# Performance work log

Hardware: AMD Instinct MI355X
Metric: run time of the kernel (lower is better)

## Reference

```python
import jax, jax.numpy as jnp
import numpy as np

N, E, F, B = 4096, 8192, 256, 16


def setup_inputs() -> dict:
    key = jax.random.key(0)
    k_x, k_idx, k_w, k_b = jax.random.split(key, 4)
    x = jax.random.normal(k_x, (B, E, F), dtype=jnp.float32)
    # Incidence matrix: each edge (column) connects 2 random distinct nodes.
    ends = jax.random.randint(k_idx, (2, E), 0, N)  # [2, E] node ids per edge
    cols = jnp.arange(E)
    inci = jnp.zeros((N, E), dtype=jnp.float32)
    inci = inci.at[ends[0], cols].set(1.0).at[ends[1], cols].set(1.0)
    w = jax.random.normal(k_w, (N, E), dtype=jnp.float32) * 0.05
    b = jax.random.normal(k_b, (N, E), dtype=jnp.float32) * 0.01
    return {"x": x, "inci": inci, "w": w, "b": b}


def reference(x, inci, w, b):
    # (w * inci + b) @ x : [N,E] x [B,E,F] -> [B,N,F]
    m = w * inci + b
    return jnp.einsum("ne,bef->bnf", m, x)
```

## Files before the change

kernel.cpp:

```cpp
#include <hip/hip_runtime.h>
#include <hip/hip_bf16.h>

#define Ndim 4096
#define Edim 8192
#define Fdim 256
#define Bdim 16
#define EB (Edim * 2)
#define NT (Edim / 64)

typedef __attribute__((ext_vector_type(8))) short bf16x8;
typedef __attribute__((ext_vector_type(4))) float f32x4;

__device__ __forceinline__ unsigned short f2bf(float f) {
  unsigned int u = __float_as_uint(f);
  u += 0x7fffu + ((u >> 16) & 1u);
  return (unsigned short)(u >> 16);
}

__device__ __forceinline__ void gload_lds16(const void* g, void* l) {
  __builtin_amdgcn_global_load_lds(
      (const __attribute__((address_space(1))) unsigned int*)g,
      (__attribute__((address_space(3))) unsigned int*)l, 16, 0, 0);
}

__device__ __forceinline__ void stage_half(const char* g, char* d) {
  gload_lds16(g, d);
  gload_lds16(g + (size_t)64 * EB, d + 8192);
}

#define RD(base, r, kk) \
  (*(const bf16x8*)((base) + (r) * 128 + ((((kk) * 64) + khi) ^ (((r) & 7) << 4))))

__global__ void convert_m(const float* __restrict__ w, const float* __restrict__ inc,
                          const float* __restrict__ bb, unsigned short* __restrict__ m) {
  size_t i = ((size_t)blockIdx.x * 256 + threadIdx.x) * 4;
  float4 wv = *(const float4*)(w + i);
  float4 iv = *(const float4*)(inc + i);
  float4 bv = *(const float4*)(bb + i);
  ushort4 o;
  o.x = f2bf(fmaf(wv.x, iv.x, bv.x));
  o.y = f2bf(fmaf(wv.y, iv.y, bv.y));
  o.z = f2bf(fmaf(wv.z, iv.z, bv.z));
  o.w = f2bf(fmaf(wv.w, iv.w, bv.w));
  *(ushort4*)(m + i) = o;
}

__global__ void transpose_x(const float* __restrict__ x, unsigned short* __restrict__ xT) {
  __shared__ unsigned short tile[64][66];
  int e0 = blockIdx.x * 64, f0 = blockIdx.y * 64, b = blockIdx.z;
  const float* xb = x + (size_t)b * Edim * Fdim;
  unsigned short* xTb = xT + (size_t)b * Fdim * Edim;
  int t = threadIdx.x;
  int fl = t & 63, rq = t >> 6;
#pragma unroll
  for (int i = 0; i < 16; i++) {
    int el = rq * 16 + i;
    float v = xb[(size_t)(e0 + el) * Fdim + f0 + fl];
    tile[el][fl] = f2bf(v);
  }
  __syncthreads();
  int ep = (t & 31) * 2;
  int fr0 = t >> 5;
#pragma unroll
  for (int j = 0; j < 8; j++) {
    int fr = fr0 + j * 8;
    unsigned int pk = (unsigned int)tile[ep][fr] | ((unsigned int)tile[ep + 1][fr] << 16);
    *(unsigned int*)&xTb[(size_t)(f0 + fr) * Edim + e0 + ep] = pk;
  }
}

template <bool S1, bool S2, bool S3, bool S4, int VM>
__device__ __forceinline__ void ktile(
    const char* lA, const char* lB,
    char* d1, const char* g1, char* d2, const char* g2,
    char* d3, const char* g3, char* d4, const char* g4,
    int lane, int wr, int wc, f32x4 acc[8][4]) {
  const int l15 = lane & 15;
  const int khi = (lane >> 4) << 4;
  bf16x8 aLo[8], aHi[8], bLo[4], bHi[4];

#pragma unroll
  for (int m = 0; m < 4; ++m)
#pragma unroll
    for (int kk = 0; kk < 2; ++kk)
      aLo[m * 2 + kk] = RD(lA, wr * 128 + m * 16 + l15, kk);
#pragma unroll
  for (int n = 0; n < 2; ++n)
#pragma unroll
    for (int kk = 0; kk < 2; ++kk)
      bLo[n * 2 + kk] = RD(lB, wc * 64 + n * 16 + l15, kk);
  if constexpr (S1) stage_half(g1, d1);
  asm volatile("s_waitcnt lgkmcnt(8)" ::: "memory");
  __builtin_amdgcn_s_barrier();
  asm volatile("s_waitcnt lgkmcnt(0)" ::: "memory");
  __builtin_amdgcn_s_setprio(1);
#pragma unroll
  for (int m = 0; m < 4; ++m)
#pragma unroll
    for (int n = 0; n < 2; ++n)
#pragma unroll
      for (int kk = 0; kk < 2; ++kk)
        acc[m][n] = __builtin_amdgcn_mfma_f32_16x16x32_bf16(aLo[m * 2 + kk], bLo[n * 2 + kk],
                                                            acc[m][n], 0, 0, 0);
  __builtin_amdgcn_s_setprio(0);
  __builtin_amdgcn_s_barrier();

#pragma unroll
  for (int n = 0; n < 2; ++n)
#pragma unroll
    for (int kk = 0; kk < 2; ++kk)
      bHi[n * 2 + kk] = RD(lB, wc * 64 + (n + 2) * 16 + l15, kk);
  if constexpr (S2) stage_half(g2, d2);
  __builtin_amdgcn_s_barrier();
  asm volatile("s_waitcnt lgkmcnt(0)" ::: "memory");
  __builtin_amdgcn_s_setprio(1);
#pragma unroll
  for (int m = 0; m < 4; ++m)
#pragma unroll
    for (int n = 0; n < 2; ++n)
#pragma unroll
      for (int kk = 0; kk < 2; ++kk)
        acc[m][n + 2] = __builtin_amdgcn_mfma_f32_16x16x32_bf16(aLo[m * 2 + kk], bHi[n * 2 + kk],
                                                                acc[m][n + 2], 0, 0, 0);
  __builtin_amdgcn_s_setprio(0);
  __builtin_amdgcn_s_barrier();

#pragma unroll
  for (int m = 0; m < 4; ++m)
#pragma unroll
    for (int kk = 0; kk < 2; ++kk)
      aHi[m * 2 + kk] = RD(lA, wr * 128 + 64 + m * 16 + l15, kk);
  if constexpr (S3) stage_half(g3, d3);
  __builtin_amdgcn_s_barrier();
  asm volatile("s_waitcnt lgkmcnt(0)" ::: "memory");
  __builtin_amdgcn_s_setprio(1);
#pragma unroll
  for (int m = 0; m < 4; ++m)
#pragma unroll
    for (int n = 0; n < 2; ++n)
#pragma unroll
      for (int kk = 0; kk < 2; ++kk)
        acc[m + 4][n] = __builtin_amdgcn_mfma_f32_16x16x32_bf16(aHi[m * 2 + kk], bLo[n * 2 + kk],
                                                                acc[m + 4][n], 0, 0, 0);
  __builtin_amdgcn_s_setprio(0);
  __builtin_amdgcn_s_barrier();

  if constexpr (S4) stage_half(g4, d4);
  __builtin_amdgcn_s_barrier();
  __builtin_amdgcn_s_setprio(1);
#pragma unroll
  for (int m = 0; m < 4; ++m)
#pragma unroll
    for (int n = 0; n < 2; ++n)
#pragma unroll
      for (int kk = 0; kk < 2; ++kk)
        acc[m + 4][n + 2] = __builtin_amdgcn_mfma_f32_16x16x32_bf16(aHi[m * 2 + kk], bHi[n * 2 + kk],
                                                                    acc[m + 4][n + 2], 0, 0, 0);
  __builtin_amdgcn_s_setprio(0);
  if constexpr (VM == 4) asm volatile("s_waitcnt vmcnt(4)" ::: "memory");
  if constexpr (VM == 0) asm volatile("s_waitcnt vmcnt(0)" ::: "memory");
  __builtin_amdgcn_s_barrier();
}

__global__ __launch_bounds__(512, 2) void gemm8(
    const unsigned short* __restrict__ A,
    const unsigned short* __restrict__ Bt,
    float* __restrict__ C) {
  __shared__ __align__(16) char smem[131072];

  const int bid = blockIdx.x;
  const int lid = ((bid & 7) << 5) | (bid >> 3);
  const int mt = lid >> 4;
  const int bb = lid & 15;

  const int tid = threadIdx.x;
  const int lane = tid & 63;
  const int w = tid >> 6;
  const int wr = w >> 2;
  const int wc = w & 3;

  const int r0 = tid >> 3;
  const int c0 = ((tid & 7) ^ (r0 & 7)) << 4;

  const char* Ag = (const char*)A + (size_t)(mt * 256) * EB + (size_t)r0 * EB + c0;
  const char* Bg = (const char*)Bt + (size_t)(bb * 256) * EB + (size_t)r0 * EB + c0;
  char* dst = smem + tid * 16;

  f32x4 acc[8][4];
#pragma unroll
  for (int m = 0; m < 8; ++m)
#pragma unroll
    for (int n = 0; n < 4; ++n) acc[m][n] = (f32x4){0.f, 0.f, 0.f, 0.f};

  const size_t HEB = (size_t)128 * EB;

  stage_half(Ag, dst);
  stage_half(Ag + HEB, dst + 16384);
  stage_half(Bg, dst + 32768);
  stage_half(Bg + HEB, dst + 49152);
  stage_half(Bg + 128, dst + 98304);
  stage_half(Bg + 128 + HEB, dst + 114688);
  asm volatile("s_waitcnt vmcnt(4)" ::: "memory");
  __builtin_amdgcn_s_barrier();

  for (int i = 0; i < NT / 2 - 1; ++i) {
    const size_t t1b = (size_t)(2 * i + 1) * 128;
    const size_t t2b = (size_t)(2 * i + 2) * 128;
    const size_t t3b = (size_t)(2 * i + 3) * 128;
    ktile<1, 1, 1, 1, 4>(smem, smem + 32768,
                         dst + 65536, Ag + t1b,
                         dst + 81920, Ag + t1b + HEB,
                         dst + 32768, Bg + t2b,
                         dst + 49152, Bg + t2b + HEB,
                         lane, wr, wc, acc);
    ktile<1, 1, 1, 1, 4>(smem + 65536, smem + 98304,
                         dst, Ag + t2b,
                         dst + 16384, Ag + t2b + HEB,
                         dst + 98304, Bg + t3b,
                         dst + 114688, Bg + t3b + HEB,
                         lane, wr, wc, acc);
  }
  {
    const size_t tlb = (size_t)(NT - 1) * 128;
    ktile<1, 1, 0, 0, 0>(smem, smem + 32768,
                         dst + 65536, Ag + tlb,
                         dst + 81920, Ag + tlb + HEB,
                         nullptr, nullptr, nullptr, nullptr,
                         lane, wr, wc, acc);
    ktile<0, 0, 0, 0, -1>(smem + 65536, smem + 98304,
                          nullptr, nullptr, nullptr, nullptr,
                          nullptr, nullptr, nullptr, nullptr,
                          lane, wr, wc, acc);
  }

  float* Cb = C + (size_t)bb * (Ndim * Fdim) + (size_t)(mt * 256) * Fdim;
#pragma unroll
  for (int m = 0; m < 8; ++m) {
    int row0 = wr * 128 + m * 16 + ((lane >> 4) << 2);
#pragma unroll
    for (int n = 0; n < 4; ++n) {
      int col = wc * 64 + n * 16 + (lane & 15);
#pragma unroll
      for (int j = 0; j < 4; ++j)
        Cb[(size_t)(row0 + j) * Fdim + col] = acc[m][n][j];
    }
  }
}

__global__ void naive_kernel(const float* __restrict__ x, const float* __restrict__ inci,
                             const float* __restrict__ w, const float* __restrict__ b,
                             float* __restrict__ out) {
  int n = blockIdx.x & (Ndim - 1);
  int bb = blockIdx.x >> 12;
  int f = threadIdx.x;
  const float* xb = x + (size_t)bb * Edim * Fdim;
  const size_t nE = (size_t)n * Edim;
  float acc = 0.f;
  for (int e = 0; e < Edim; e++) {
    float m = fmaf(w[nE + e], inci[nE + e], b[nE + e]);
    acc = fmaf(m, xb[(size_t)e * Fdim + f], acc);
  }
  out[(size_t)bb * Ndim * Fdim + (size_t)n * Fdim + f] = acc;
}

extern "C" void kernel_launch(void* const* d_in, const int* in_sizes, int n_in,
                              void* d_out, int out_size, void* d_ws, size_t ws_size,
                              hipStream_t stream) {
  const float* x = (const float*)d_in[0];
  const float* inci = (const float*)d_in[1];
  const float* w = (const float*)d_in[2];
  const float* b = (const float*)d_in[3];
  float* out = (float*)d_out;

  size_t mBytes = (size_t)Ndim * Edim * 2;
  size_t xTBytes = (size_t)Bdim * Fdim * Edim * 2;
  if (ws_size >= mBytes + xTBytes) {
    unsigned short* m_bf = (unsigned short*)d_ws;
    unsigned short* xT = m_bf + (size_t)Ndim * Edim;
    convert_m<<<(Ndim * (size_t)Edim) / 4 / 256, 256, 0, stream>>>(w, inci, b, m_bf);
    transpose_x<<<dim3(Edim / 64, Fdim / 64, Bdim), 256, 0, stream>>>(x, xT);
    gemm8<<<256, 512, 0, stream>>>(m_bf, xT, out);
  } else {
    naive_kernel<<<Bdim * Ndim, 256, 0, stream>>>(x, inci, w, b, out);
  }
}
```

Baseline: 334.4 us.

## Prefetch next tile's A fragments into registers across ktile boundaries

Restructures the per-tile GEMM pipeline so the low half of A for the next K-tile is read from LDS during the last MFMA phase of the current tile and carried in registers. The B low/high fragments are now loaded together up front, and the explicit lgkmcnt waits are dropped in favour of compiler-managed waits. The vmcnt waits are also moved earlier. The goal is to hide LDS read latency behind MFMA work and to cut stalls at phase boundaries, at the cost of more live VGPRs and a reordered barrier/stage schedule that could expose new hazards.

```diff
diff --git a/kernel.cpp b/kernel.cpp
--- a/kernel.cpp
+++ b/kernel.cpp
@@ -30,6 +30,8 @@
 
 #define RD(base, r, kk) \
   (*(const bf16x8*)((base) + (r) * 128 + ((((kk) * 64) + khi) ^ (((r) & 7) << 4))))
+
+#define BAR() do { __builtin_amdgcn_s_barrier(); asm volatile("" ::: "memory"); } while (0)
 
 __global__ void convert_m(const float* __restrict__ w, const float* __restrict__ inc,
                           const float* __restrict__ bb, unsigned short* __restrict__ m) {
@@ -69,70 +71,61 @@
   }
 }
 
-template <bool S1, bool S2, bool S3, bool S4, int VM>
+template <int MODE>
 __device__ __forceinline__ void ktile(
-    const char* lA, const char* lB,
+    const char* lA, const char* lB, const char* lAn,
     char* d1, const char* g1, char* d2, const char* g2,
     char* d3, const char* g3, char* d4, const char* g4,
-    int lane, int wr, int wc, f32x4 acc[8][4]) {
+    int lane, int wr, int wc, bf16x8 (&aCur)[8], f32x4 acc[8][4]) {
   const int l15 = lane & 15;
   const int khi = (lane >> 4) << 4;
-  bf16x8 aLo[8], aHi[8], bLo[4], bHi[4];
-
-#pragma unroll
-  for (int m = 0; m < 4; ++m)
-#pragma unroll
-    for (int kk = 0; kk < 2; ++kk)
-      aLo[m * 2 + kk] = RD(lA, wr * 128 + m * 16 + l15, kk);
+  bf16x8 bLo[4], bHi[4], aHi[8];
+
+  if constexpr (MODE >= 1) stage_half(g1, d1);
+  BAR();
 #pragma unroll
   for (int n = 0; n < 2; ++n)
 #pragma unroll
     for (int kk = 0; kk < 2; ++kk)
       bLo[n * 2 + kk] = RD(lB, wc * 64 + n * 16 + l15, kk);
-  if constexpr (S1) stage_half(g1, d1);
-  asm volatile("s_waitcnt lgkmcnt(8)" ::: "memory");
-  __builtin_amdgcn_s_barrier();
-  asm volatile("s_waitcnt lgkmcnt(0)" ::: "memory");
-  __builtin_amdgcn_s_setprio(1);
-#pragma unroll
-  for (int m = 0; m < 4; ++m)
-#pragma unroll
-    for (int n = 0; n < 2; ++n)
-#pragma unroll
-      for (int kk = 0; kk < 2; ++kk)
-        acc[m][n] = __builtin_amdgcn_mfma_f32_16x16x32_bf16(aLo[m * 2 + kk], bLo[n * 2 + kk],
+#pragma unroll
+  for (int n = 0; n < 2; ++n)
+#pragma unroll
+    for (int kk = 0; kk < 2; ++kk)
+      bHi[n * 2 + kk] = RD(lB, wc * 64 + (n + 2) * 16 + l15, kk);
+  __builtin_amdgcn_s_setprio(1);
+#pragma unroll
+  for (int m = 0; m < 4; ++m)
+#pragma unroll
+    for (int n = 0; n < 2; ++n)
+#pragma unroll
+      for (int kk = 0; kk < 2; ++kk)
+        acc[m][n] = __builtin_amdgcn_mfma_f32_16x16x32_bf16(aCur[m * 2 + kk], bLo[n * 2 + kk],
                                                             acc[m][n], 0, 0, 0);
   __builtin_amdgcn_s_setprio(0);
-  __builtin_amdgcn_s_barrier();
-
-#pragma unroll
-  for (int n = 0; n < 2; ++n)
-#pragma unroll
-    for (int kk = 0; kk < 2; ++kk)
-      bHi[n * 2 + kk] = RD(lB, wc * 64 + (n + 2) * 16 + l15, kk);
-  if constexpr (S2) stage_half(g2, d2);
-  __builtin_amdgcn_s_barrier();
-  asm volatile("s_waitcnt lgkmcnt(0)" ::: "memory");
-  __builtin_amdgcn_s_setprio(1);
-#pragma unroll
-  for (int m = 0; m < 4; ++m)
-#pragma unroll
-    for (int n = 0; n < 2; ++n)
-#pragma unroll
-      for (int kk = 0; kk < 2; ++kk)
-        acc[m][n + 2] = __builtin_amdgcn_mfma_f32_16x16x32_bf16(aLo[m * 2 + kk], bHi[n * 2 + kk],
+  BAR();
+
+  if constexpr (MODE >= 1) stage_half(g2, d2);
+  BAR();
+#pragma unroll
+  for (int m = 0; m < 4; ++m)
+#pragma unroll
+    for (int kk = 0; kk < 2; ++kk)
+      aHi[m * 2 + kk] = RD(lA, wr * 128 + 64 + m * 16 + l15, kk);
+  __builtin_amdgcn_s_setprio(1);
+#pragma unroll
+  for (int m = 0; m < 4; ++m)
+#pragma unroll
+    for (int n = 0; n < 2; ++n)
+#pragma unroll
+      for (int kk = 0; kk < 2; ++kk)
+        acc[m][n + 2] = __builtin_amdgcn_mfma_f32_16x16x32_bf16(aCur[m * 2 + kk], bHi[n * 2 + kk],
                                                                 acc[m][n + 2], 0, 0, 0);
   __builtin_amdgcn_s_setprio(0);
-  __builtin_amdgcn_s_barrier();
-
-#pragma unroll
-  for (int m = 0; m < 4; ++m)
-#pragma unroll
-    for (int kk = 0; kk < 2; ++kk)
-      aHi[m * 2 + kk] = RD(lA, wr * 128 + 64 + m * 16 + l15, kk);
-  if constexpr (S3) stage_half(g3, d3);
-  __builtin_amdgcn_s_barrier();
-  asm volatile("s_waitcnt lgkmcnt(0)" ::: "memory");
+  BAR();
+
+  if constexpr (MODE == 2) stage_half(g3, d3);
+  BAR();
   __builtin_amdgcn_s_setprio(1);
 #pragma unroll
   for (int m = 0; m < 4; ++m)
@@ -143,10 +136,19 @@
         acc[m + 4][n] = __builtin_amdgcn_mfma_f32_16x16x32_bf16(aHi[m * 2 + kk], bLo[n * 2 + kk],
                                                                 acc[m + 4][n], 0, 0, 0);
   __builtin_amdgcn_s_setprio(0);
-  __builtin_amdgcn_s_barrier();
-
-  if constexpr (S4) stage_half(g4, d4);
-  __builtin_amdgcn_s_barrier();
+  if constexpr (MODE == 2) asm volatile("s_waitcnt vmcnt(2)" ::: "memory");
+  if constexpr (MODE == 1) asm volatile("s_waitcnt vmcnt(0)" ::: "memory");
+  BAR();
+
+  if constexpr (MODE == 2) stage_half(g4, d4);
+  BAR();
+  if constexpr (MODE >= 1) {
+#pragma unroll
+    for (int m = 0; m < 4; ++m)
+#pragma unroll
+      for (int kk = 0; kk < 2; ++kk)
+        aCur[m * 2 + kk] = RD(lAn, wr * 128 + m * 16 + l15, kk);
+  }
   __builtin_amdgcn_s_setprio(1);
 #pragma unroll
   for (int m = 0; m < 4; ++m)
@@ -157,9 +159,7 @@
         acc[m + 4][n + 2] = __builtin_amdgcn_mfma_f32_16x16x32_bf16(aHi[m * 2 + kk], bHi[n * 2 + kk],
                                                                     acc[m + 4][n + 2], 0, 0, 0);
   __builtin_amdgcn_s_setprio(0);
-  if constexpr (VM == 4) asm volatile("s_waitcnt vmcnt(4)" ::: "memory");
-  if constexpr (VM == 0) asm volatile("s_waitcnt vmcnt(0)" ::: "memory");
-  __builtin_amdgcn_s_barrier();
+  BAR();
 }
 
 __global__ __launch_bounds__(512, 2) void gemm8(
@@ -178,6 +178,8 @@
   const int w = tid >> 6;
   const int wr = w >> 2;
   const int wc = w & 3;
+  const int l15 = lane & 15;
+  const int khi = (lane >> 4) << 4;
 
   const int r0 = tid >> 3;
   const int c0 = ((tid & 7) ^ (r0 & 7)) << 4;
@@ -201,36 +203,43 @@
   stage_half(Bg + 128, dst + 98304);
   stage_half(Bg + 128 + HEB, dst + 114688);
   asm volatile("s_waitcnt vmcnt(4)" ::: "memory");
-  __builtin_amdgcn_s_barrier();
+  BAR();
+
+  bf16x8 aCur[8];
+#pragma unroll
+  for (int m = 0; m < 4; ++m)
+#pragma unroll
+    for (int kk = 0; kk < 2; ++kk)
+      aCur[m * 2 + kk] = RD((const char*)smem, wr * 128 + m * 16 + l15, kk);
 
   for (int i = 0; i < NT / 2 - 1; ++i) {
     const size_t t1b = (size_t)(2 * i + 1) * 128;
     const size_t t2b = (size_t)(2 * i + 2) * 128;
     const size_t t3b = (size_t)(2 * i + 3) * 128;
-    ktile<1, 1, 1, 1, 4>(smem, smem + 32768,
-                         dst + 65536, Ag + t1b,
-                         dst + 81920, Ag + t1b + HEB,
-                         dst + 32768, Bg + t2b,
-                         dst + 49152, Bg + t2b + HEB,
-                         lane, wr, wc, acc);
-    ktile<1, 1, 1, 1, 4>(smem + 65536, smem + 98304,
-                         dst, Ag + t2b,
-                         dst + 16384, Ag + t2b + HEB,
-                         dst + 98304, Bg + t3b,
-                         dst + 114688, Bg + t3b + HEB,
-                         lane, wr, wc, acc);
+    ktile<2>(smem, smem + 32768, smem + 65536,
+             dst + 65536, Ag + t1b,
+             dst + 81920, Ag + t1b + HEB,
+             dst + 32768, Bg + t2b,
+             dst + 49152, Bg + t2b + HEB,
+             lane, wr, wc, aCur, acc);
+    ktile<2>(smem + 65536, smem + 98304, smem,
+             dst, Ag + t2b,
+             dst + 16384, Ag + t2b + HEB,
+             dst + 98304, Bg + t3b,
+             dst + 114688, Bg + t3b + HEB,
+             lane, wr, wc, aCur, acc);
   }
   {
     const size_t tlb = (size_t)(NT - 1) * 128;
-    ktile<1, 1, 0, 0, 0>(smem, smem + 32768,
-                         dst + 65536, Ag + tlb,
-                         dst + 81920, Ag + tlb + HEB,
-                         nullptr, nullptr, nullptr, nullptr,
-                         lane, wr, wc, acc);
-    ktile<0, 0, 0, 0, -1>(smem + 65536, smem + 98304,
-                          nullptr, nullptr, nullptr, nullptr,
-                          nullptr, nullptr, nullptr, nullptr,
-                          lane, wr, wc, acc);
+    ktile<1>(smem, smem + 32768, smem + 65536,
+             dst + 65536, Ag + tlb,
+             dst + 81920, Ag + tlb + HEB,
+             nullptr, nullptr, nullptr, nullptr,
+             lane, wr, wc, aCur, acc);
+    ktile<0>(smem + 65536, smem + 98304, nullptr,
+             nullptr, nullptr, nullptr, nullptr,
+             nullptr, nullptr, nullptr, nullptr,
+             lane, wr, wc, aCur, acc);
   }
 
   float* Cb = C + (size_t)bb * (Ndim * Fdim) + (size_t)(mt * 256) * Fdim;
```

Measured after the change: 778.5 us. +132.8%, slower.
